# Kernel optimization log

Hardware: AMD Instinct MI355X
Metric: run time of the kernel (lower is better)

## Reference

```python
import jax, jax.numpy as jnp
import numpy as np

N_NODES = 100000
N_EDGES = 640000
IN_D = 128
OUT_D = 128


def setup_inputs() -> dict:
    key = jax.random.key(0)
    k_x, k_ei, k_ws, k_wn = jax.random.split(key, 4)
    scale = 1.0 / np.sqrt(IN_D)
    return {
        "x": jax.random.normal(k_x, (N_NODES, IN_D), dtype=jnp.float32),
        "ei": jax.random.randint(k_ei, (2, N_EDGES), 0, N_NODES, dtype=jnp.int64),
        "Ws": jax.random.normal(k_ws, (IN_D, OUT_D), dtype=jnp.float32) * scale,
        "bs": jnp.zeros((OUT_D,), dtype=jnp.float32),
        "Wn": jax.random.normal(k_wn, (IN_D, OUT_D), dtype=jnp.float32) * scale,
        "bn": jnp.zeros((OUT_D,), dtype=jnp.float32),
    }


def reference(x, ei, Ws, bs, Wn, bn):
    # x: [N, in_d], ei: [2, E]
    src, dst = ei[0], ei[1]
    n = x.shape[0]
    # scatter-sum of gathered source features onto destinations
    agg = jax.ops.segment_sum(x[src], dst, num_segments=n)  # [N, in_d]
    # in-degree per destination node
    deg = jax.ops.segment_sum(jnp.ones(src.shape[0], dtype=x.dtype), dst, num_segments=n)  # [N]
    agg = agg / jnp.maximum(deg, 1.0)[:, None]
    # dual linear + relu (dropout is identity in eval)
    return jax.nn.relu(x @ Ws + bs + agg @ Wn + bn)
```

## Files before the change

kernel.cpp:

```cpp
#include <hip/hip_runtime.h>
#include <hip/hip_bf16.h>

#define D 128

typedef __attribute__((ext_vector_type(8))) short short8v;
typedef __attribute__((ext_vector_type(4))) float f32x4;

__device__ __forceinline__ short f2bf(float f) {
    union { float f; unsigned u; } v;
    v.f = f;
    unsigned u = v.u;
    unsigned r = (u + 0x7FFFu + ((u >> 16) & 1u)) >> 16;
    return (short)r;
}

__device__ __forceinline__ float bf2f(unsigned u16) {
    union { unsigned u; float f; } v;
    v.u = u16 << 16;
    return v.f;
}

__device__ __forceinline__ unsigned pkbf2(float lo, float hi) {
    __hip_bfloat162 h = __float22bfloat162_rn(make_float2(lo, hi));
    union { __hip_bfloat162 h; unsigned u; } v;
    v.h = h;
    return v.u;
}

__global__ __launch_bounds__(256) void hist_kernel(const int* __restrict__ dst,
                                                   int* __restrict__ counts, int nE) {
    int e = blockIdx.x * 256 + threadIdx.x;
    if (e < nE) atomicAdd(&counts[dst[e]], 1);
}

__global__ __launch_bounds__(256) void scan_partial_kernel(const int* __restrict__ counts,
                                                           int* __restrict__ bsums, int n) {
    __shared__ int wsum[4];
    const int t = threadIdx.x;
    const int i0 = blockIdx.x * 1024 + t * 4;
    int s = 0;
#pragma unroll
    for (int j = 0; j < 4; ++j) s += (i0 + j < n) ? counts[i0 + j] : 0;
#pragma unroll
    for (int off = 32; off > 0; off >>= 1) s += __shfl_down(s, off, 64);
    if ((t & 63) == 0) wsum[t >> 6] = s;
    __syncthreads();
    if (t == 0) bsums[blockIdx.x] = wsum[0] + wsum[1] + wsum[2] + wsum[3];
}

__global__ __launch_bounds__(128) void scan_bsums_kernel(const int* __restrict__ bsums,
                                                         int* __restrict__ ebsums,
                                                         int* __restrict__ rowptr_n,
                                                         int nb) {
    __shared__ int sh[128];
    const int t = threadIdx.x;
    int v = (t < nb) ? bsums[t] : 0;
    sh[t] = v;
    __syncthreads();
    for (int off = 1; off < 128; off <<= 1) {
        int u = (t >= off) ? sh[t - off] : 0;
        __syncthreads();
        sh[t] += u;
        __syncthreads();
    }
    if (t < nb) ebsums[t] = sh[t] - v;
    if (t == 127) *rowptr_n = sh[127];
}

__global__ __launch_bounds__(256) void scan_final_kernel(int* __restrict__ counts,
                                                         const int* __restrict__ ebsums,
                                                         int* __restrict__ rowptr, int n) {
    __shared__ int sh[256];
    const int t = threadIdx.x;
    const int i0 = blockIdx.x * 1024 + t * 4;
    int c[4];
    int s = 0;
#pragma unroll
    for (int j = 0; j < 4; ++j) {
        c[j] = (i0 + j < n) ? counts[i0 + j] : 0;
        s += c[j];
    }
    sh[t] = s;
    __syncthreads();
    for (int off = 1; off < 256; off <<= 1) {
        int u = (t >= off) ? sh[t - off] : 0;
        __syncthreads();
        sh[t] += u;
        __syncthreads();
    }
    int run = ebsums[blockIdx.x] + sh[t] - s;
#pragma unroll
    for (int j = 0; j < 4; ++j) {
        int i = i0 + j;
        if (i < n) {
            rowptr[i] = run;
            counts[i] = run;
            run += c[j];
        }
    }
}

__global__ __launch_bounds__(256) void fill_kernel(const int* __restrict__ src,
                                                   const int* __restrict__ dst,
                                                   int* __restrict__ cursor,
                                                   int* __restrict__ csr, int nE) {
    int e = blockIdx.x * 256 + threadIdx.x;
    if (e < nE) {
        int pos = atomicAdd(&cursor[dst[e]], 1);
        csr[pos] = src[e];
    }
}

__global__ __launch_bounds__(256) void wt_pack_kernel(const float* __restrict__ Ws,
                                                      const float* __restrict__ Wn,
                                                      short* __restrict__ WT) {
    int idx = blockIdx.x * 256 + threadIdx.x;
    int nn = idx >> 7;
    int k = idx & (D - 1);
    float v = (nn < D) ? Ws[k * D + nn] : Wn[k * D + (nn - D)];
    WT[idx] = f2bf(v);
}

__global__ __launch_bounds__(256) void gemm_mfma_kernel(const float* __restrict__ x,
                                                        const short* __restrict__ WT,
                                                        const float* __restrict__ bs,
                                                        const float* __restrict__ bn,
                                                        float* __restrict__ outS,
                                                        unsigned short* __restrict__ hNb,
                                                        int nStrips) {
    const int wave = threadIdx.x >> 6;
    const int lane = threadIdx.x & 63;
    const int lrow = lane & 15;
    const int ko = (lane >> 4) * 8;
    const bool isS = (wave < 2);

    short8v b[4][4];
#pragma unroll
    for (int j = 0; j < 4; ++j) {
        const int ct = wave * 4 + j;
        const short* __restrict__ wp = WT + (size_t)(ct * 16 + lrow) * D + ko;
#pragma unroll
        for (int ks = 0; ks < 4; ++ks)
            b[j][ks] = *reinterpret_cast<const short8v*>(wp + ks * 32);
    }

    float bias[4];
#pragma unroll
    for (int j = 0; j < 4; ++j) {
        int c = ((wave & 1) * 4 + j) * 16 + lrow;
        bias[j] = isS ? (bs[c] + bn[c]) : 0.f;
    }

    const int stride = gridDim.x;

    auto loadA = [&](int strip, float4* fa) {
        const float* __restrict__ xr = x + ((size_t)strip * 16 + lrow) * D + ko;
#pragma unroll
        for (int s = 0; s < 4; ++s) {
            fa[2 * s] = *reinterpret_cast<const float4*>(xr + s * 32);
            fa[2 * s + 1] = *reinterpret_cast<const float4*>(xr + s * 32 + 4);
        }
    };

    auto compute = [&](int strip, const float4* cur) {
        short8v a[4];
#pragma unroll
        for (int s = 0; s < 4; ++s) {
            const float4 lo = cur[2 * s], hi = cur[2 * s + 1];
            union { short8v s8; unsigned u[4]; } af;
            af.u[0] = pkbf2(lo.x, lo.y);
            af.u[1] = pkbf2(lo.z, lo.w);
            af.u[2] = pkbf2(hi.x, hi.y);
            af.u[3] = pkbf2(hi.z, hi.w);
            a[s] = af.s8;
        }
        f32x4 acc[4];
#pragma unroll
        for (int j = 0; j < 4; ++j) acc[j] = (f32x4){0.f, 0.f, 0.f, 0.f};
#pragma unroll
        for (int j = 0; j < 4; ++j)
#pragma unroll
            for (int ks = 0; ks < 4; ++ks)
                acc[j] = __builtin_amdgcn_mfma_f32_16x16x32_bf16(a[ks], b[j][ks], acc[j], 0, 0, 0);

        const int r0 = strip * 16 + (lane >> 4) * 4;
        if (isS) {
#pragma unroll
            for (int j = 0; j < 4; ++j) {
                int c = ((wave & 1) * 4 + j) * 16 + lrow;
#pragma unroll
                for (int rg = 0; rg < 4; ++rg)
                    outS[(size_t)(r0 + rg) * D + c] = acc[j][rg] + bias[j];
            }
        } else {
#pragma unroll
            for (int j = 0; j < 4; ++j) {
                int c = ((wave & 1) * 4 + j) * 16 + lrow;
#pragma unroll
                for (int rg = 0; rg < 4; ++rg)
                    hNb[(size_t)(r0 + rg) * D + c] = (unsigned short)f2bf(acc[j][rg]);
            }
        }
    };

    float4 faA[8], faB[8];
    int strip = blockIdx.x;
    if (strip >= nStrips) return;
    loadA(strip, faA);
    for (; strip < nStrips; strip += 2 * stride) {
        const int s1 = strip + stride;
        if (s1 < nStrips) loadA(s1, faB);
        compute(strip, faA);
        if (s1 < nStrips) {
            const int s2 = s1 + stride;
            if (s2 < nStrips) loadA(s2, faA);
            compute(s1, faB);
        }
    }
}

__global__ __launch_bounds__(256) void gather_kernel(const int* __restrict__ rowptr,
                                                     const int* __restrict__ csr,
                                                     const unsigned short* __restrict__ hNb,
                                                     float* __restrict__ out, int n) {
    const int wave = threadIdx.x >> 6;
    const int lane = threadIdx.x & 63;
    const int d = blockIdx.x * 4 + wave;
    if (d >= n) return;

    const int beg = rowptr[d];
    const int end = rowptr[d + 1];
    float ax = 0.f, ay = 0.f;

    int i = beg;
    for (; i + 3 < end; i += 4) {
        int s0 = csr[i], s1 = csr[i + 1], s2 = csr[i + 2], s3 = csr[i + 3];
        unsigned v0 = *reinterpret_cast<const unsigned*>(hNb + (size_t)s0 * D + lane * 2);
        unsigned v1 = *reinterpret_cast<const unsigned*>(hNb + (size_t)s1 * D + lane * 2);
        unsigned v2 = *reinterpret_cast<const unsigned*>(hNb + (size_t)s2 * D + lane * 2);
        unsigned v3 = *reinterpret_cast<const unsigned*>(hNb + (size_t)s3 * D + lane * 2);
        ax += (bf2f(v0 & 0xffffu) + bf2f(v1 & 0xffffu)) +
              (bf2f(v2 & 0xffffu) + bf2f(v3 & 0xffffu));
        ay += (bf2f(v0 >> 16) + bf2f(v1 >> 16)) + (bf2f(v2 >> 16) + bf2f(v3 >> 16));
    }
    for (; i < end; ++i) {
        int s0 = csr[i];
        unsigned v0 = *reinterpret_cast<const unsigned*>(hNb + (size_t)s0 * D + lane * 2);
        ax += bf2f(v0 & 0xffffu);
        ay += bf2f(v0 >> 16);
    }

    const float inv = 1.0f / fmaxf((float)(end - beg), 1.0f);
    float2 o = *reinterpret_cast<const float2*>(out + (size_t)d * D + lane * 2);
    o.x = fmaxf(fmaf(ax, inv, o.x), 0.f);
    o.y = fmaxf(fmaf(ay, inv, o.y), 0.f);
    *reinterpret_cast<float2*>(out + (size_t)d * D + lane * 2) = o;
}

extern "C" void kernel_launch(void* const* d_in, const int* in_sizes, int n_in,
                              void* d_out, int out_size, void* d_ws, size_t ws_size,
                              hipStream_t stream) {
    const float* x  = (const float*)d_in[0];
    const int*   ei = (const int*)d_in[1];
    const float* Ws = (const float*)d_in[2];
    const float* bs = (const float*)d_in[3];
    const float* Wn = (const float*)d_in[4];
    const float* bn = (const float*)d_in[5];
    float* out = (float*)d_out;

    const int n  = in_sizes[0] / D;
    const int nE = in_sizes[1] / 2;
    const int* src = ei;
    const int* dst = ei + nE;
    const int nb = (n + 1023) / 1024;

    unsigned short* hNb = (unsigned short*)d_ws;
    short* WT    = (short*)(hNb + (size_t)n * D);
    int*   counts = (int*)(WT + 256 * D);
    int*   rowptr = counts + n;
    int*   csr    = rowptr + n + 1;
    int*   bsums  = csr + nE;
    int*   ebsums = bsums + 128;

    hipMemsetAsync(counts, 0, (size_t)n * sizeof(int), stream);
    hist_kernel<<<(nE + 255) / 256, 256, 0, stream>>>(dst, counts, nE);
    scan_partial_kernel<<<nb, 256, 0, stream>>>(counts, bsums, n);
    scan_bsums_kernel<<<1, 128, 0, stream>>>(bsums, ebsums, rowptr + n, nb);
    scan_final_kernel<<<nb, 256, 0, stream>>>(counts, ebsums, rowptr, n);
    fill_kernel<<<(nE + 255) / 256, 256, 0, stream>>>(src, dst, counts, csr, nE);

    wt_pack_kernel<<<(256 * D) / 256, 256, 0, stream>>>(Ws, Wn, WT);
    const int nStrips = (n + 15) / 16;
    const int gGrid = nStrips < 1024 ? nStrips : 1024;
    gemm_mfma_kernel<<<gGrid, 256, 0, stream>>>(x, WT, bs, bn, out, hNb, nStrips);

    gather_kernel<<<(n + 3) / 4, 256, 0, stream>>>(rowptr, csr, hNb, out, n);
}
```

Measured before the change: 169.9 us.

## Aggregate raw features before GEMM and fuse dual linear with concatenated K

```diff
diff --git a/kernel.cpp b/kernel.cpp
--- a/kernel.cpp
+++ b/kernel.cpp
@@ -14,12 +14,6 @@
     return (short)r;
 }
 
-__device__ __forceinline__ float bf2f(unsigned u16) {
-    union { unsigned u; float f; } v;
-    v.u = u16 << 16;
-    return v.f;
-}
-
 __device__ __forceinline__ unsigned pkbf2(float lo, float hi) {
     __hip_bfloat162 h = __float22bfloat162_rn(make_float2(lo, hi));
     union { __hip_bfloat162 h; unsigned u; } v;
@@ -27,10 +21,23 @@
     return v.u;
 }
 
-__global__ __launch_bounds__(256) void hist_kernel(const int* __restrict__ dst,
-                                                   int* __restrict__ counts, int nE) {
-    int e = blockIdx.x * 256 + threadIdx.x;
-    if (e < nE) atomicAdd(&counts[dst[e]], 1);
+__global__ __launch_bounds__(256) void prep_kernel(const int* __restrict__ dst,
+                                                   int* __restrict__ counts, int nE,
+                                                   const float* __restrict__ Ws,
+                                                   const float* __restrict__ Wn,
+                                                   short* __restrict__ WT2) {
+    const int nbE = (nE + 255) >> 8;
+    const int b = blockIdx.x;
+    if (b < nbE) {
+        int e = b * 256 + threadIdx.x;
+        if (e < nE) atomicAdd(&counts[dst[e]], 1);
+    } else {
+        int idx = (b - nbE) * 256 + threadIdx.x;
+        int nn = idx >> 8;
+        int k = idx & 255;
+        float v = (k < D) ? Ws[k * D + nn] : Wn[(k - D) * D + nn];
+        WT2[idx] = f2bf(v);
+    }
 }
 
 __global__ __launch_bounds__(256) void scan_partial_kernel(const int* __restrict__ counts,
@@ -111,150 +118,131 @@
     }
 }
 
-__global__ __launch_bounds__(256) void wt_pack_kernel(const float* __restrict__ Ws,
-                                                      const float* __restrict__ Wn,
-                                                      short* __restrict__ WT) {
-    int idx = blockIdx.x * 256 + threadIdx.x;
-    int nn = idx >> 7;
-    int k = idx & (D - 1);
-    float v = (nn < D) ? Ws[k * D + nn] : Wn[k * D + (nn - D)];
-    WT[idx] = f2bf(v);
-}
-
-__global__ __launch_bounds__(256) void gemm_mfma_kernel(const float* __restrict__ x,
-                                                        const short* __restrict__ WT,
-                                                        const float* __restrict__ bs,
-                                                        const float* __restrict__ bn,
-                                                        float* __restrict__ outS,
-                                                        unsigned short* __restrict__ hNb,
-                                                        int nStrips) {
+__global__ __launch_bounds__(256) void gather_kernel(const int* __restrict__ rowptr,
+                                                     const int* __restrict__ csr,
+                                                     const float* __restrict__ x,
+                                                     unsigned short* __restrict__ aggb,
+                                                     int n) {
+    const int wave = threadIdx.x >> 6;
+    const int lane = threadIdx.x & 63;
+    const int d = blockIdx.x * 4 + wave;
+    if (d >= n) return;
+
+    const int beg = rowptr[d];
+    const int end = rowptr[d + 1];
+    float ax = 0.f, ay = 0.f;
+
+    int i = beg;
+    for (; i + 3 < end; i += 4) {
+        int s0 = csr[i], s1 = csr[i + 1], s2 = csr[i + 2], s3 = csr[i + 3];
+        float2 v0 = *reinterpret_cast<const float2*>(x + (size_t)s0 * D + lane * 2);
+        float2 v1 = *reinterpret_cast<const float2*>(x + (size_t)s1 * D + lane * 2);
+        float2 v2 = *reinterpret_cast<const float2*>(x + (size_t)s2 * D + lane * 2);
+        float2 v3 = *reinterpret_cast<const float2*>(x + (size_t)s3 * D + lane * 2);
+        ax += (v0.x + v1.x) + (v2.x + v3.x);
+        ay += (v0.y + v1.y) + (v2.y + v3.y);
+    }
+    for (; i < end; ++i) {
+        int s0 = csr[i];
+        float2 v0 = *reinterpret_cast<const float2*>(x + (size_t)s0 * D + lane * 2);
+        ax += v0.x;
+        ay += v0.y;
+    }
+
+    const float inv = 1.0f / fmaxf((float)(end - beg), 1.0f);
+    *reinterpret_cast<unsigned*>(aggb + (size_t)d * D + lane * 2) = pkbf2(ax * inv, ay * inv);
+}
+
+__global__ __launch_bounds__(256) void gemm_fused_kernel(const float* __restrict__ x,
+                                                         const short* __restrict__ WT2,
+                                                         const float* __restrict__ bs,
+                                                         const float* __restrict__ bn,
+                                                         const unsigned short* __restrict__ aggb,
+                                                         float* __restrict__ out,
+                                                         int n, int nStrips) {
     const int wave = threadIdx.x >> 6;
     const int lane = threadIdx.x & 63;
     const int lrow = lane & 15;
     const int ko = (lane >> 4) * 8;
-    const bool isS = (wave < 2);
-
-    short8v b[4][4];
-#pragma unroll
-    for (int j = 0; j < 4; ++j) {
-        const int ct = wave * 4 + j;
-        const short* __restrict__ wp = WT + (size_t)(ct * 16 + lrow) * D + ko;
-#pragma unroll
-        for (int ks = 0; ks < 4; ++ks)
+
+    short8v b[2][8];
+#pragma unroll
+    for (int j = 0; j < 2; ++j) {
+        const short* __restrict__ wp = WT2 + (size_t)((wave * 2 + j) * 16 + lrow) * 256 + ko;
+#pragma unroll
+        for (int ks = 0; ks < 8; ++ks)
             b[j][ks] = *reinterpret_cast<const short8v*>(wp + ks * 32);
     }
-
-    float bias[4];
-#pragma unroll
-    for (int j = 0; j < 4; ++j) {
-        int c = ((wave & 1) * 4 + j) * 16 + lrow;
-        bias[j] = isS ? (bs[c] + bn[c]) : 0.f;
+    float bias[2];
+#pragma unroll
+    for (int j = 0; j < 2; ++j) {
+        int c = (wave * 2 + j) * 16 + lrow;
+        bias[j] = bs[c] + bn[c];
     }
 
     const int stride = gridDim.x;
 
-    auto loadA = [&](int strip, float4* fa) {
-        const float* __restrict__ xr = x + ((size_t)strip * 16 + lrow) * D + ko;
-#pragma unroll
-        for (int s = 0; s < 4; ++s) {
-            fa[2 * s] = *reinterpret_cast<const float4*>(xr + s * 32);
-            fa[2 * s + 1] = *reinterpret_cast<const float4*>(xr + s * 32 + 4);
+    auto loadA = [&](int strip, float4* fx, short8v* ag) {
+        const size_t row = (size_t)min(strip * 16 + lrow, n - 1);
+        const float* __restrict__ xr = x + row * D + ko;
+        const unsigned short* __restrict__ ar = aggb + row * D + ko;
+#pragma unroll
+        for (int ks = 0; ks < 4; ++ks) {
+            fx[2 * ks] = *reinterpret_cast<const float4*>(xr + ks * 32);
+            fx[2 * ks + 1] = *reinterpret_cast<const float4*>(xr + ks * 32 + 4);
+            ag[ks] = *reinterpret_cast<const short8v*>(ar + ks * 32);
         }
     };
 
-    auto compute = [&](int strip, const float4* cur) {
-        short8v a[4];
-#pragma unroll
-        for (int s = 0; s < 4; ++s) {
-            const float4 lo = cur[2 * s], hi = cur[2 * s + 1];
+    auto compute = [&](int strip, const float4* fx, const short8v* ag) {
+        short8v a[8];
+#pragma unroll
+        for (int ks = 0; ks < 4; ++ks) {
+            const float4 lo = fx[2 * ks], hi = fx[2 * ks + 1];
             union { short8v s8; unsigned u[4]; } af;
             af.u[0] = pkbf2(lo.x, lo.y);
             af.u[1] = pkbf2(lo.z, lo.w);
             af.u[2] = pkbf2(hi.x, hi.y);
             af.u[3] = pkbf2(hi.z, hi.w);
-            a[s] = af.s8;
-        }
-        f32x4 acc[4];
-#pragma unroll
-        for (int j = 0; j < 4; ++j) acc[j] = (f32x4){0.f, 0.f, 0.f, 0.f};
-#pragma unroll
-        for (int j = 0; j < 4; ++j)
-#pragma unroll
-            for (int ks = 0; ks < 4; ++ks)
+            a[ks] = af.s8;
+            a[ks + 4] = ag[ks];
+        }
+        f32x4 acc[2];
+        acc[0] = (f32x4){0.f, 0.f, 0.f, 0.f};
+        acc[1] = (f32x4){0.f, 0.f, 0.f, 0.f};
+#pragma unroll
+        for (int j = 0; j < 2; ++j)
+#pragma unroll
+            for (int ks = 0; ks < 8; ++ks)
                 acc[j] = __builtin_amdgcn_mfma_f32_16x16x32_bf16(a[ks], b[j][ks], acc[j], 0, 0, 0);
 
         const int r0 = strip * 16 + (lane >> 4) * 4;
-        if (isS) {
-#pragma unroll
-            for (int j = 0; j < 4; ++j) {
-                int c = ((wave & 1) * 4 + j) * 16 + lrow;
-#pragma unroll
-                for (int rg = 0; rg < 4; ++rg)
-                    outS[(size_t)(r0 + rg) * D + c] = acc[j][rg] + bias[j];
+#pragma unroll
+        for (int j = 0; j < 2; ++j) {
+            const int c = (wave * 2 + j) * 16 + lrow;
+#pragma unroll
+            for (int rg = 0; rg < 4; ++rg) {
+                int r = r0 + rg;
+                if (r < n) out[(size_t)r * D + c] = fmaxf(acc[j][rg] + bias[j], 0.f);
             }
-        } else {
-#pragma unroll
-            for (int j = 0; j < 4; ++j) {
-                int c = ((wave & 1) * 4 + j) * 16 + lrow;
-#pragma unroll
-                for (int rg = 0; rg < 4; ++rg)
-                    hNb[(size_t)(r0 + rg) * D + c] = (unsigned short)f2bf(acc[j][rg]);
-            }
         }
     };
 
-    float4 faA[8], faB[8];
+    float4 fxA[8], fxB[8];
+    short8v agA[4], agB[4];
     int strip = blockIdx.x;
     if (strip >= nStrips) return;
-    loadA(strip, faA);
+    loadA(strip, fxA, agA);
     for (; strip < nStrips; strip += 2 * stride) {
         const int s1 = strip + stride;
-        if (s1 < nStrips) loadA(s1, faB);
-        compute(strip, faA);
+        if (s1 < nStrips) loadA(s1, fxB, agB);
+        compute(strip, fxA, agA);
         if (s1 < nStrips) {
             const int s2 = s1 + stride;
-            if (s2 < nStrips) loadA(s2, faA);
-            compute(s1, faB);
-        }
-    }
-}
-
-__global__ __launch_bounds__(256) void gather_kernel(const int* __restrict__ rowptr,
-                                                     const int* __restrict__ csr,
-                                                     const unsigned short* __restrict__ hNb,
-                                                     float* __restrict__ out, int n) {
-    const int wave = threadIdx.x >> 6;
-    const int lane = threadIdx.x & 63;
-    const int d = blockIdx.x * 4 + wave;
-    if (d >= n) return;
-
-    const int beg = rowptr[d];
-    const int end = rowptr[d + 1];
-    float ax = 0.f, ay = 0.f;
-
-    int i = beg;
-    for (; i + 3 < end; i += 4) {
-        int s0 = csr[i], s1 = csr[i + 1], s2 = csr[i + 2], s3 = csr[i + 3];
-        unsigned v0 = *reinterpret_cast<const unsigned*>(hNb + (size_t)s0 * D + lane * 2);
-        unsigned v1 = *reinterpret_cast<const unsigned*>(hNb + (size_t)s1 * D + lane * 2);
-        unsigned v2 = *reinterpret_cast<const unsigned*>(hNb + (size_t)s2 * D + lane * 2);
-        unsigned v3 = *reinterpret_cast<const unsigned*>(hNb + (size_t)s3 * D + lane * 2);
-        ax += (bf2f(v0 & 0xffffu) + bf2f(v1 & 0xffffu)) +
-              (bf2f(v2 & 0xffffu) + bf2f(v3 & 0xffffu));
-        ay += (bf2f(v0 >> 16) + bf2f(v1 >> 16)) + (bf2f(v2 >> 16) + bf2f(v3 >> 16));
-    }
-    for (; i < end; ++i) {
-        int s0 = csr[i];
-        unsigned v0 = *reinterpret_cast<const unsigned*>(hNb + (size_t)s0 * D + lane * 2);
-        ax += bf2f(v0 & 0xffffu);
-        ay += bf2f(v0 >> 16);
-    }
-
-    const float inv = 1.0f / fmaxf((float)(end - beg), 1.0f);
-    float2 o = *reinterpret_cast<const float2*>(out + (size_t)d * D + lane * 2);
-    o.x = fmaxf(fmaf(ax, inv, o.x), 0.f);
-    o.y = fmaxf(fmaf(ay, inv, o.y), 0.f);
-    *reinterpret_cast<float2*>(out + (size_t)d * D + lane * 2) = o;
+            if (s2 < nStrips) loadA(s2, fxA, agA);
+            compute(s1, fxB, agB);
+        }
+    }
 }
 
 extern "C" void kernel_launch(void* const* d_in, const int* in_sizes, int n_in,
@@ -274,25 +262,26 @@
     const int* dst = ei + nE;
     const int nb = (n + 1023) / 1024;
 
-    unsigned short* hNb = (unsigned short*)d_ws;
-    short* WT    = (short*)(hNb + (size_t)n * D);
-    int*   counts = (int*)(WT + 256 * D);
+    unsigned short* aggb = (unsigned short*)d_ws;
+    short* WT2   = (short*)(aggb + (size_t)n * D);
+    int*   counts = (int*)(WT2 + (size_t)D * 256);
     int*   rowptr = counts + n;
     int*   csr    = rowptr + n + 1;
     int*   bsums  = csr + nE;
     int*   ebsums = bsums + 128;
 
+    const int nbE = (nE + 255) / 256;
+
     hipMemsetAsync(counts, 0, (size_t)n * sizeof(int), stream);
-    hist_kernel<<<(nE + 255) / 256, 256, 0, stream>>>(dst, counts, nE);
+    prep_kernel<<<nbE + 128, 256, 0, stream>>>(dst, counts, nE, Ws, Wn, WT2);
     scan_partial_kernel<<<nb, 256, 0, stream>>>(counts, bsums, n);
     scan_bsums_kernel<<<1, 128, 0, stream>>>(bsums, ebsums, rowptr + n, nb);
     scan_final_kernel<<<nb, 256, 0, stream>>>(counts, ebsums, rowptr, n);
     fill_kernel<<<(nE + 255) / 256, 256, 0, stream>>>(src, dst, counts, csr, nE);
 
-    wt_pack_kernel<<<(256 * D) / 256, 256, 0, stream>>>(Ws, Wn, WT);
+    gather_kernel<<<(n + 3) / 4, 256, 0, stream>>>(rowptr, csr, x, aggb, n);
+
     const int nStrips = (n + 15) / 16;
     const int gGrid = nStrips < 1024 ? nStrips : 1024;
-    gemm_mfma_kernel<<<gGrid, 256, 0, stream>>>(x, WT, bs, bn, out, hNb, nStrips);
-
-    gather_kernel<<<(n + 3) / 4, 256, 0, stream>>>(rowptr, csr, hNb, out, n);
-}
+    gemm_fused_kernel<<<gGrid, 256, 0, stream>>>(x, WT2, bs, bn, aggb, out, n, nStrips);
+}
```

Measured after the change: 179.2 us. 5.5% more time.
